# Performance work log

Hardware: AMD Instinct MI355X
Metric: run time of the kernel (lower is better)

## Reference

```python
import jax, jax.numpy as jnp
import numpy as np

B, T, D_IN, D_OUT = 4, 2048, 1024, 1024


def setup_inputs() -> dict:
    key = jax.random.key(0)
    k1, k2, k3, k4 = jax.random.split(key, 4)
    s_in = 1.0 / np.sqrt(D_IN)
    return {
        "input_vector": jax.random.normal(k1, (B, T, D_IN), dtype=jnp.float32),
        "w_q": jax.random.normal(k2, (D_IN, D_OUT), dtype=jnp.float32) * s_in,
        "w_k": jax.random.normal(k3, (D_IN, D_OUT), dtype=jnp.float32) * s_in,
        "w_v": jax.random.normal(k4, (D_IN, D_OUT), dtype=jnp.float32) * s_in,
    }


def reference(input_vector, w_q, w_k, w_v):
    # projections: [B, T, D_OUT]
    q = jnp.einsum("btd,de->bte", input_vector, w_q)
    k = jnp.einsum("btd,de->bte", input_vector, w_k)
    v = jnp.einsum("btd,de->bte", input_vector, w_v)

    T_ = q.shape[1]
    # raw scores [B, T, T]
    scores = jnp.einsum("bqd,bkd->bqk", q, k)
    # causal mask (strict upper triangle masked to -inf), applied BEFORE scaling
    # (as in the original; -inf is invariant under the scale anyway)
    causal = jnp.tril(jnp.ones((T_, T_), dtype=bool))  # True = keep
    scores = jnp.where(causal[None, :, :], scores, -jnp.inf)
    scores = scores / jnp.sqrt(jnp.asarray(k.shape[-1], scores.dtype))
    attn = jax.nn.softmax(scores, axis=-1)
    # dropout = 0.0 (eval): identity
    return jnp.einsum("bqk,bkd->bqd", attn, v)
```

## Files before the change

kernel.cpp:

```cpp
#include <hip/hip_runtime.h>
#include <cstdint>

typedef unsigned short u16;
typedef __attribute__((ext_vector_type(8))) short short8;
typedef __attribute__((ext_vector_type(16))) float f32x16;

__device__ __forceinline__ u16 f2bf(float f) {
  uint32_t u = __float_as_uint(f);
  u += 0x7FFFu + ((u >> 16) & 1u);
  return (u16)(u >> 16);
}

__device__ __forceinline__ void async_ld16(u16* lds, const u16* g) {
  __builtin_amdgcn_global_load_lds((const __attribute__((address_space(1))) uint32_t*)g,
                                   (__attribute__((address_space(3))) uint32_t*)lds,
                                   16, 0, 0);
}

__device__ __forceinline__ void lgkm0_fence() {
  asm volatile("s_waitcnt lgkmcnt(0)" ::: "memory");
  __builtin_amdgcn_sched_barrier(0);
}
__device__ __forceinline__ void vmw6_fence() {
  asm volatile("s_waitcnt vmcnt(6)" ::: "memory");
  __builtin_amdgcn_sched_barrier(0);
}
__device__ __forceinline__ void vmw0_fence() {
  asm volatile("s_waitcnt vmcnt(0)" ::: "memory");
  __builtin_amdgcn_sched_barrier(0);
}

#define MFMA32 __builtin_amdgcn_mfma_f32_32x32x16_bf16

template <int ROLE>
__global__ __launch_bounds__(512, 2) void g8(
    const u16* __restrict__ Xbf, const u16* __restrict__ Wt,
    u16* __restrict__ QK, u16* __restrict__ VtAll,
    u16* __restrict__ P, float* __restrict__ lpart)
{
  const int b = blockIdx.x;
  const int tid = threadIdx.x;
  const int lane = tid & 63;
  const int wave = tid >> 6;
  const int wr2 = wave >> 2;
  const int wc2 = wave & 3;
  const int m32 = lane & 31;
  const int hh = lane >> 5;

  __shared__ __align__(16) u16 ls[2][2][16384];

  const u16 *A, *B;
  u16* C = nullptr;
  long ldc = 1024;
  int m0, n0, zb = 0, nt = 0;

  if constexpr (ROLE == 0) {
    if (b < 256) {
      const int mat = b >> 7, v = b & 127;
      m0 = (v >> 2) * 256;
      n0 = (v & 3) * 256;
      A = Xbf;
      B = Wt + (long)mat * 1024 * 1024;
      C = QK + (long)mat * 8192 * 1024;
      ldc = 1024;
    } else {
      const int v = b - 256;
      m0 = (v >> 5) * 256;
      n0 = (v & 31) * 256;
      A = Wt + 2L * 1024 * 1024;
      B = Xbf;
      C = VtAll;
      ldc = 8192;
    }
  } else {
    zb = b / 36;
    const int w = b - zb * 36;
    int mt = 0;
    while ((mt + 1) * (mt + 2) / 2 <= w) ++mt;
    nt = w - mt * (mt + 1) / 2;
    m0 = mt * 256;
    n0 = nt * 256;
    A = QK + (long)zb * 2048 * 1024;
    B = QK + 8192L * 1024 + (long)zb * 2048 * 1024;
  }

  const int sr = tid >> 3, sg = tid & 7;
  const u16* pAst = A + (long)(m0 + sr) * 1024 + ((sg ^ (sr & 7)) * 8);
  const u16* pBst = B + (long)(n0 + sr) * 1024 + ((sg ^ (sr & 7)) * 8);

#define STG_A(bf, h, t_) do { \
    u16* _d = &ls[bf][0][(h) * 8192] + tid * 8; \
    const u16* _s = pAst + (long)(h) * 131072 + (long)(t_) * 64; \
    async_ld16(_d, _s); async_ld16(_d + 4096, _s + 65536); } while (0)
#define STG_B(bf, h, t_) do { \
    u16* _d = &ls[bf][1][(h) * 8192] + tid * 8; \
    const u16* _s = pBst + (long)(h) * 131072 + (long)(t_) * 64; \
    async_ld16(_d, _s); async_ld16(_d + 4096, _s + 65536); } while (0)

  int offAk[4], offBk[4];
#pragma unroll
  for (int ks = 0; ks < 4; ++ks) {
    const int kq = ((ks << 1) | hh) ^ (m32 & 7);
    offAk[ks] = (wr2 * 128 + m32) * 64 + kq * 8;
    offBk[ks] = (wc2 * 64 + m32) * 64 + kq * 8;
  }

  f32x16 acc[4][2];
#pragma unroll
  for (int i = 0; i < 4; ++i)
#pragma unroll
    for (int j = 0; j < 2; ++j)
#pragma unroll
      for (int r = 0; r < 16; ++r) acc[i][j][r] = 0.f;

  STG_A(0, 0, 0); STG_A(0, 1, 0); STG_B(0, 0, 0); STG_B(0, 1, 0);
  STG_B(1, 0, 1); STG_B(1, 1, 1); STG_A(1, 0, 1);
  vmw6_fence();
  __builtin_amdgcn_s_barrier();

  short8 A0[4], A1[4], A2[4], A3[4], B0r[4], B1r[4];

#pragma unroll 1
  for (int t = 0; t < 16; ++t) {
    const u16* la = ls[t & 1][0];
    const u16* lb = ls[t & 1][1];

#pragma unroll
    for (int ks = 0; ks < 4; ++ks) {
      A0[ks]  = *(const short8*)&la[offAk[ks]];
      A1[ks]  = *(const short8*)&la[offAk[ks] + 2048];
      B0r[ks] = *(const short8*)&lb[offBk[ks]];
    }
    if (t < 15) STG_A((t + 1) & 1, 1, t + 1);
    __builtin_amdgcn_s_barrier();
    lgkm0_fence();
    __builtin_amdgcn_s_setprio(1);
#pragma unroll
    for (int ks = 0; ks < 4; ++ks) {
      acc[0][0] = MFMA32(A0[ks], B0r[ks], acc[0][0], 0, 0, 0);
      acc[1][0] = MFMA32(A1[ks], B0r[ks], acc[1][0], 0, 0, 0);
    }
    __builtin_amdgcn_s_setprio(0);
    __builtin_amdgcn_s_barrier();

#pragma unroll
    for (int ks = 0; ks < 4; ++ks)
      B1r[ks] = *(const short8*)&lb[offBk[ks] + 2048];
    __builtin_amdgcn_s_barrier();
    lgkm0_fence();
    __builtin_amdgcn_s_setprio(1);
#pragma unroll
    for (int ks = 0; ks < 4; ++ks) {
      acc[0][1] = MFMA32(A0[ks], B1r[ks], acc[0][1], 0, 0, 0);
      acc[1][1] = MFMA32(A1[ks], B1r[ks], acc[1][1], 0, 0, 0);
    }
    __builtin_amdgcn_s_setprio(0);
    __builtin_amdgcn_s_barrier();

#pragma unroll
    for (int ks = 0; ks < 4; ++ks) {
      A2[ks] = *(const short8*)&la[offAk[ks] + 4096];
      A3[ks] = *(const short8*)&la[offAk[ks] + 6144];
    }
    if (t < 14) STG_B(t & 1, 0, t + 2);
    __builtin_amdgcn_s_barrier();
    lgkm0_fence();
    __builtin_amdgcn_s_setprio(1);
#pragma unroll
    for (int ks = 0; ks < 4; ++ks) {
      acc[2][0] = MFMA32(A2[ks], B0r[ks], acc[2][0], 0, 0, 0);
      acc[3][0] = MFMA32(A3[ks], B0r[ks], acc[3][0], 0, 0, 0);
    }
    __builtin_amdgcn_s_setprio(0);
    __builtin_amdgcn_s_barrier();

    if (t < 14) { STG_B(t & 1, 1, t + 2); STG_A(t & 1, 0, t + 2); }
    __builtin_amdgcn_s_barrier();
    __builtin_amdgcn_s_setprio(1);
#pragma unroll
    for (int ks = 0; ks < 4; ++ks) {
      acc[2][1] = MFMA32(A2[ks], B1r[ks], acc[2][1], 0, 0, 0);
      acc[3][1] = MFMA32(A3[ks], B1r[ks], acc[3][1], 0, 0, 0);
    }
    __builtin_amdgcn_s_setprio(0);
    if (t < 14) vmw6_fence(); else vmw0_fence();
    __builtin_amdgcn_s_barrier();
  }
#undef STG_A
#undef STG_B

  const int ec = lane & 31;
  const int rb = hh * 4;

  if constexpr (ROLE == 0) {
#pragma unroll
    for (int i = 0; i < 4; ++i) {
      const int rbase = m0 + wr2 * 128 + i * 32 + rb;
#pragma unroll
      for (int j = 0; j < 2; ++j) {
        const int col = n0 + wc2 * 64 + j * 32 + ec;
#pragma unroll
        for (int r = 0; r < 16; ++r) {
          const int row = rbase + (r & 3) + 8 * (r >> 2);
          C[(long)row * ldc + col] = f2bf(acc[i][j][r]);
        }
      }
    }
  } else {
    u16* Cp = P + (long)zb * 2048 * 2048;
    float* lp = lpart + (long)zb * 32 * 2048 + (long)(nt * 4 + wc2) * 2048;
#pragma unroll
    for (int i = 0; i < 4; ++i) {
      const int rbl = wr2 * 128 + i * 32 + rb;
      float rsum[16];
#pragma unroll
      for (int r = 0; r < 16; ++r) rsum[r] = 0.f;
#pragma unroll
      for (int j = 0; j < 2; ++j) {
        const int col = n0 + wc2 * 64 + j * 32 + ec;
#pragma unroll
        for (int r = 0; r < 16; ++r) {
          const int row = m0 + rbl + (r & 3) + 8 * (r >> 2);
          float pv = __expf(acc[i][j][r] * 0.03125f);
          if (col > row) pv = 0.f;
          Cp[(long)row * 2048 + col] = f2bf(pv);
          rsum[r] += pv;
        }
      }
#pragma unroll
      for (int r = 0; r < 16; ++r) {
        float s = rsum[r];
#pragma unroll
        for (int off = 1; off < 32; off <<= 1) s += __shfl_xor(s, off, 64);
        if ((lane & 31) == 0)
          lp[m0 + rbl + (r & 3) + 8 * (r >> 2)] = s;
      }
    }
  }
}

template <int ROLE>
__global__ __launch_bounds__(256) void gk(
    const u16* __restrict__ Xbf, const u16* __restrict__ Wt,
    u16* __restrict__ QK, u16* __restrict__ VtAll,
    u16* __restrict__ P, float* __restrict__ lpart,
    float* __restrict__ out)
{
  const int b = blockIdx.x;
  const int tid = threadIdx.x;
  const int lane = tid & 63;
  const int wave = tid >> 6;
  const int wr = (wave >> 1) * 64;
  const int wc = (wave & 1) * 64;

  __shared__ __align__(16) u16 ls[4][4096];
  __shared__ float l_s[128];

  const int c0 = tid, c1 = tid + 256;
  const int r0 = c0 >> 2, q0 = ((c0 & 3) ^ ((c0 >> 3) & 3)) * 8;
  const int r1 = c1 >> 2, q1 = ((c1 & 3) ^ ((c1 >> 3) & 3)) * 8;

  const int m32 = lane & 31;
  const int hh = lane >> 5;
  const int rsw = (m32 >> 1) & 3;
  int offA[2][2], offB[2][2];
#pragma unroll
  for (int i = 0; i < 2; ++i)
#pragma unroll
    for (int ks = 0; ks < 2; ++ks) {
      const int kq = ((ks << 1) | hh) ^ rsw;
      offA[i][ks] = (wr + i * 32 + m32) * 32 + kq * 8;
      offB[i][ks] = (wc + i * 32 + m32) * 32 + kq * 8;
    }

  const u16 *A, *B;
  int lda, ldb, kmax, m0, n0, mb, nb, zb = 0;
  const int u = b & 7, idx = b >> 3;
  zb = blockIdx.y;
  if (idx < 8) { mb = 15 - u; nb = idx; }
  else         { mb = u;      nb = idx - 8; }
  A = P + (long)zb * 2048 * 2048; lda = 2048;
  B = VtAll + (long)zb * 2048; ldb = 8192;
  kmax = (mb + 1) * 128;
  m0 = mb * 128;
  n0 = nb * 128;

  const u16* pA0 = A + (long)(m0 + r0) * lda + q0;
  const u16* pA1 = A + (long)(m0 + r1) * lda + q1;
  const u16* pB0 = B + (long)(n0 + r0) * ldb + q0;
  const u16* pB1 = B + (long)(n0 + r1) * ldb + q1;

  f32x16 acc[2][2];
#pragma unroll
  for (int i = 0; i < 2; ++i)
#pragma unroll
    for (int j = 0; j < 2; ++j)
#pragma unroll
      for (int r = 0; r < 16; ++r) acc[i][j][r] = 0.f;

  async_ld16(&ls[0][c0 * 8], pA0);
  async_ld16(&ls[0][c1 * 8], pA1);
  async_ld16(&ls[2][c0 * 8], pB0);
  async_ld16(&ls[2][c1 * 8], pB1);
  pA0 += 32; pA1 += 32; pB0 += 32; pB1 += 32;

  int p = 0;
  for (int k0 = 0; k0 < kmax; k0 += 32) {
    __syncthreads();
    if (k0 + 32 < kmax) {
      u16* la = ls[p ^ 1];
      u16* lb = ls[2 + (p ^ 1)];
      async_ld16(&la[c0 * 8], pA0);
      async_ld16(&la[c1 * 8], pA1);
      async_ld16(&lb[c0 * 8], pB0);
      async_ld16(&lb[c1 * 8], pB1);
      pA0 += 32; pA1 += 32; pB0 += 32; pB1 += 32;
    }

    const u16* la = ls[p];
    const u16* lb = ls[2 + p];
#pragma unroll
    for (int ks = 0; ks < 2; ++ks) {
      const short8 a0 = *(const short8*)&la[offA[0][ks]];
      const short8 a1 = *(const short8*)&la[offA[1][ks]];
      const short8 b0 = *(const short8*)&lb[offB[0][ks]];
      const short8 b1 = *(const short8*)&lb[offB[1][ks]];
      acc[0][0] = MFMA32(a0, b0, acc[0][0], 0, 0, 0);
      acc[0][1] = MFMA32(a0, b1, acc[0][1], 0, 0, 0);
      acc[1][0] = MFMA32(a1, b0, acc[1][0], 0, 0, 0);
      acc[1][1] = MFMA32(a1, b1, acc[1][1], 0, 0, 0);
    }
    p ^= 1;
  }

  const int ec = lane & 31;
  const int rb = (lane >> 5) * 4;

  __syncthreads();
  if (tid < 128) {
    const float* lp = lpart + (long)zb * 32 * 2048 + m0 + tid;
    float s0 = 0.f, s1 = 0.f;
    const int nch = 2 * (mb + 1);
    for (int c = 0; c < nch; c += 2) {
      s0 += lp[(long)c * 2048];
      s1 += lp[(long)(c + 1) * 2048];
    }
    l_s[tid] = 1.f / (s0 + s1);
  }
  __syncthreads();
  float* Cf = out + (long)zb * 2048 * 1024;
#pragma unroll
  for (int i = 0; i < 2; ++i) {
    const int rbl = wr + i * 32 + rb;
#pragma unroll
    for (int j = 0; j < 2; ++j) {
      const int col = n0 + wc + j * 32 + ec;
#pragma unroll
      for (int r = 0; r < 16; ++r) {
        const int rl = rbl + (r & 3) + 8 * (r >> 2);
        Cf[(long)(m0 + rl) * 1024 + col] = acc[i][j][r] * l_s[rl];
      }
    }
  }
}

__global__ __launch_bounds__(256) void cast_fused(
    const float* __restrict__ x, const float* __restrict__ w0,
    const float* __restrict__ w1, const float* __restrict__ w2,
    u16* __restrict__ Xbf, u16* __restrict__ Wt)
{
  const int b = blockIdx.x;
  if (b < 8192) {
    const long i = ((long)b * 256 + threadIdx.x) * 4;
    const float4 v = *(const float4*)(x + i);
    ushort4 o;
    o.x = f2bf(v.x); o.y = f2bf(v.y); o.z = f2bf(v.z); o.w = f2bf(v.w);
    *(ushort4*)(Xbf + i) = o;
  } else {
    const int bb = b - 8192;
    const int z = bb >> 10, rem = bb & 1023;
    const float* W = (z == 0) ? w0 : (z == 1) ? w1 : w2;
    u16* o = Wt + (long)z * 1024 * 1024;
    __shared__ float t[32][33];
    const int n0 = (rem & 31) * 32, k0 = (rem >> 5) * 32;
    const int tx = threadIdx.x & 31, ty = threadIdx.x >> 5;
    for (int r = ty; r < 32; r += 8) t[r][tx] = W[(long)(k0 + r) * 1024 + n0 + tx];
    __syncthreads();
    for (int r = ty; r < 32; r += 8) o[(long)(n0 + r) * 1024 + k0 + tx] = f2bf(t[tx][r]);
  }
}

extern "C" void kernel_launch(void* const* d_in, const int* in_sizes, int n_in,
                              void* d_out, int out_size, void* d_ws, size_t ws_size,
                              hipStream_t stream) {
  const float* X  = (const float*)d_in[0];
  const float* Wq = (const float*)d_in[1];
  const float* Wk = (const float*)d_in[2];
  const float* Wv = (const float*)d_in[3];
  float* out = (float*)d_out;

  u16* Xbf   = (u16*)d_ws;
  u16* Wt    = Xbf + 8192L * 1024;
  u16* QK    = Wt + 3L * 1024 * 1024;
  u16* VtAll = QK + 2L * 8192 * 1024;
  u16* P     = VtAll + 1024L * 8192;
  float* lpart = (float*)(P + 4L * 2048 * 2048);

  cast_fused<<<8192 + 3072, 256, 0, stream>>>(X, Wq, Wk, Wv, Xbf, Wt);

  g8<0><<<384, 512, 0, stream>>>(Xbf, Wt, QK, VtAll, P, lpart);

  g8<1><<<144, 512, 0, stream>>>(Xbf, Wt, QK, VtAll, P, lpart);

  gk<2><<<dim3(128, 4), 256, 0, stream>>>(Xbf, Wt, QK, VtAll, P, lpart, out);
}
```

Before: 255.3 us.

## Rebalance kernels: fuse Q/K projection tiles, co-schedule V with scores, shrink PV tiles

The Q and K projections now share one A tile of X per block, each block loading both weight matrices, so X is read once for both outputs. The V-transpose projection moves into the scores launch, so the 144 causal score blocks and 128 V blocks run together and fill the GPU better. Score tiles are computed transposed so P can be written with 4-wide vector stores, and the row-sum partials shrink to one per 128-key chunk. The PV kernel uses 128x64 output tiles ordered heaviest-first to improve occupancy and load balance, at the cost of re-reading P once more per extra column tile.

```diff
diff --git a/kernel.cpp b/kernel.cpp
--- a/kernel.cpp
+++ b/kernel.cpp
@@ -49,44 +49,49 @@
 
   __shared__ __align__(16) u16 ls[2][2][16384];
 
-  const u16 *A, *B;
-  u16* C = nullptr;
-  long ldc = 1024;
-  int m0, n0, zb = 0, nt = 0;
+  const u16 *Abase, *Bh0, *Bh1;
+  int m0, n0, zb = 0;
+  bool scoresRole = false;
 
   if constexpr (ROLE == 0) {
-    if (b < 256) {
-      const int mat = b >> 7, v = b & 127;
-      m0 = (v >> 2) * 256;
-      n0 = (v & 3) * 256;
-      A = Xbf;
-      B = Wt + (long)mat * 1024 * 1024;
-      C = QK + (long)mat * 8192 * 1024;
-      ldc = 1024;
+    m0 = (b >> 3) * 256;
+    n0 = (b & 7) * 128;
+    Abase = Xbf;
+    Bh0 = Wt;
+    Bh1 = Wt + 1024L * 1024;
+  } else {
+    if (b < 144) {
+      scoresRole = true;
+      zb = b / 36;
+      const int w = b - zb * 36;
+      int mt = 0;
+      while ((mt + 1) * (mt + 2) / 2 <= w) ++mt;
+      const int nt = w - mt * (mt + 1) / 2;
+      m0 = nt * 256;
+      n0 = mt * 256;
+      Abase = QK + 8192L * 1024 + (long)zb * 2048 * 1024;
+      const u16* Bq = QK + (long)zb * 2048 * 1024;
+      Bh0 = Bq; Bh1 = Bq;
     } else {
-      const int v = b - 256;
+      const int v = b - 144;
       m0 = (v >> 5) * 256;
       n0 = (v & 31) * 256;
-      A = Wt + 2L * 1024 * 1024;
-      B = Xbf;
-      C = VtAll;
-      ldc = 8192;
-    }
+      Abase = Wt + 2L * 1024 * 1024;
+      Bh0 = Xbf; Bh1 = Xbf;
+    }
+  }
+
+  const int sr = tid >> 3, sg = tid & 7;
+  const long swz = (long)((sg ^ (sr & 7)) * 8);
+  const u16* pAst = Abase + (long)(m0 + sr) * 1024 + swz;
+  const u16* pB[2];
+  if constexpr (ROLE == 0) {
+    pB[0] = Bh0 + (long)(n0 + sr) * 1024 + swz;
+    pB[1] = Bh1 + (long)(n0 + sr) * 1024 + swz;
   } else {
-    zb = b / 36;
-    const int w = b - zb * 36;
-    int mt = 0;
-    while ((mt + 1) * (mt + 2) / 2 <= w) ++mt;
-    nt = w - mt * (mt + 1) / 2;
-    m0 = mt * 256;
-    n0 = nt * 256;
-    A = QK + (long)zb * 2048 * 1024;
-    B = QK + 8192L * 1024 + (long)zb * 2048 * 1024;
-  }
-
-  const int sr = tid >> 3, sg = tid & 7;
-  const u16* pAst = A + (long)(m0 + sr) * 1024 + ((sg ^ (sr & 7)) * 8);
-  const u16* pBst = B + (long)(n0 + sr) * 1024 + ((sg ^ (sr & 7)) * 8);
+    pB[0] = Bh0 + (long)(n0 + sr) * 1024 + swz;
+    pB[1] = Bh0 + (long)(n0 + 128 + sr) * 1024 + swz;
+  }
 
 #define STG_A(bf, h, t_) do { \
     u16* _d = &ls[bf][0][(h) * 8192] + tid * 8; \
@@ -94,15 +99,20 @@
     async_ld16(_d, _s); async_ld16(_d + 4096, _s + 65536); } while (0)
 #define STG_B(bf, h, t_) do { \
     u16* _d = &ls[bf][1][(h) * 8192] + tid * 8; \
-    const u16* _s = pBst + (long)(h) * 131072 + (long)(t_) * 64; \
+    const u16* _s = pB[h] + (long)(t_) * 64; \
     async_ld16(_d, _s); async_ld16(_d + 4096, _s + 65536); } while (0)
 
-  int offAk[4], offBk[4];
+  int offAk[4], offBk[2][4];
 #pragma unroll
   for (int ks = 0; ks < 4; ++ks) {
     const int kq = ((ks << 1) | hh) ^ (m32 & 7);
     offAk[ks] = (wr2 * 128 + m32) * 64 + kq * 8;
-    offBk[ks] = (wc2 * 64 + m32) * 64 + kq * 8;
+#pragma unroll
+    for (int j = 0; j < 2; ++j) {
+      const int rowB = (ROLE == 0) ? (j * 128 + wc2 * 32 + m32)
+                                   : (wc2 * 64 + j * 32 + m32);
+      offBk[j][ks] = rowB * 64 + kq * 8;
+    }
   }
 
   f32x16 acc[4][2];
@@ -129,7 +139,7 @@
     for (int ks = 0; ks < 4; ++ks) {
       A0[ks]  = *(const short8*)&la[offAk[ks]];
       A1[ks]  = *(const short8*)&la[offAk[ks] + 2048];
-      B0r[ks] = *(const short8*)&lb[offBk[ks]];
+      B0r[ks] = *(const short8*)&lb[offBk[0][ks]];
     }
     if (t < 15) STG_A((t + 1) & 1, 1, t + 1);
     __builtin_amdgcn_s_barrier();
@@ -145,7 +155,7 @@
 
 #pragma unroll
     for (int ks = 0; ks < 4; ++ks)
-      B1r[ks] = *(const short8*)&lb[offBk[ks] + 2048];
+      B1r[ks] = *(const short8*)&lb[offBk[1][ks]];
     __builtin_amdgcn_s_barrier();
     lgkm0_fence();
     __builtin_amdgcn_s_setprio(1);
@@ -194,6 +204,52 @@
 
   if constexpr (ROLE == 0) {
 #pragma unroll
+    for (int j = 0; j < 2; ++j) {
+      u16* Cj = QK + (long)j * 8192 * 1024;
+      const int col = n0 + wc2 * 32 + ec;
+#pragma unroll
+      for (int i = 0; i < 4; ++i) {
+        const int rbase = m0 + wr2 * 128 + i * 32 + rb;
+#pragma unroll
+        for (int r = 0; r < 16; ++r) {
+          const int row = rbase + (r & 3) + 8 * (r >> 2);
+          Cj[(long)row * 1024 + col] = f2bf(acc[i][j][r]);
+        }
+      }
+    }
+  } else if (scoresRole) {
+    u16* Pp = P + (long)zb * 2048 * 2048;
+    float* lpz = lpart + (long)zb * 16 * 2048;
+    const int chunk = (m0 >> 7) + wr2;
+#pragma unroll
+    for (int j = 0; j < 2; ++j) {
+      const int q = n0 + wc2 * 64 + j * 32 + ec;
+      float s = 0.f;
+#pragma unroll
+      for (int i = 0; i < 4; ++i) {
+        const int kb = m0 + wr2 * 128 + i * 32 + rb;
+#pragma unroll
+        for (int u = 0; u < 4; ++u) {
+          const int k0r = kb + u * 8;
+          float pv[4];
+#pragma unroll
+          for (int v = 0; v < 4; ++v) {
+            float e = __expf(acc[i][j][u * 4 + v] * 0.03125f);
+            if (k0r + v > q) e = 0.f;
+            pv[v] = e;
+            s += e;
+          }
+          ushort4 o;
+          o.x = f2bf(pv[0]); o.y = f2bf(pv[1]);
+          o.z = f2bf(pv[2]); o.w = f2bf(pv[3]);
+          *(ushort4*)&Pp[(long)q * 2048 + k0r] = o;
+        }
+      }
+      s += __shfl_xor(s, 32, 64);
+      if (hh == 0) lpz[(long)chunk * 2048 + q] = s;
+    }
+  } else {
+#pragma unroll
     for (int i = 0; i < 4; ++i) {
       const int rbase = m0 + wr2 * 128 + i * 32 + rb;
 #pragma unroll
@@ -202,59 +258,37 @@
 #pragma unroll
         for (int r = 0; r < 16; ++r) {
           const int row = rbase + (r & 3) + 8 * (r >> 2);
-          C[(long)row * ldc + col] = f2bf(acc[i][j][r]);
+          VtAll[(long)row * 8192 + col] = f2bf(acc[i][j][r]);
         }
       }
     }
-  } else {
-    u16* Cp = P + (long)zb * 2048 * 2048;
-    float* lp = lpart + (long)zb * 32 * 2048 + (long)(nt * 4 + wc2) * 2048;
-#pragma unroll
-    for (int i = 0; i < 4; ++i) {
-      const int rbl = wr2 * 128 + i * 32 + rb;
-      float rsum[16];
-#pragma unroll
-      for (int r = 0; r < 16; ++r) rsum[r] = 0.f;
-#pragma unroll
-      for (int j = 0; j < 2; ++j) {
-        const int col = n0 + wc2 * 64 + j * 32 + ec;
-#pragma unroll
-        for (int r = 0; r < 16; ++r) {
-          const int row = m0 + rbl + (r & 3) + 8 * (r >> 2);
-          float pv = __expf(acc[i][j][r] * 0.03125f);
-          if (col > row) pv = 0.f;
-          Cp[(long)row * 2048 + col] = f2bf(pv);
-          rsum[r] += pv;
-        }
-      }
-#pragma unroll
-      for (int r = 0; r < 16; ++r) {
-        float s = rsum[r];
-#pragma unroll
-        for (int off = 1; off < 32; off <<= 1) s += __shfl_xor(s, off, 64);
-        if ((lane & 31) == 0)
-          lp[m0 + rbl + (r & 3) + 8 * (r >> 2)] = s;
-      }
-    }
-  }
-}
-
-template <int ROLE>
-__global__ __launch_bounds__(256) void gk(
-    const u16* __restrict__ Xbf, const u16* __restrict__ Wt,
-    u16* __restrict__ QK, u16* __restrict__ VtAll,
-    u16* __restrict__ P, float* __restrict__ lpart,
-    float* __restrict__ out)
+  }
+}
+
+__global__ __launch_bounds__(256) void pv(
+    const u16* __restrict__ VtAll, const u16* __restrict__ P,
+    const float* __restrict__ lpart, float* __restrict__ out)
 {
   const int b = blockIdx.x;
   const int tid = threadIdx.x;
   const int lane = tid & 63;
   const int wave = tid >> 6;
   const int wr = (wave >> 1) * 64;
-  const int wc = (wave & 1) * 64;
-
-  __shared__ __align__(16) u16 ls[4][4096];
+  const int wc = (wave & 1) * 32;
+
+  __shared__ __align__(16) u16 lsa[2][4096];
+  __shared__ __align__(16) u16 lsb[2][2048];
   __shared__ float l_s[128];
+
+  const int zb = blockIdx.y;
+  const int mb = 15 - (b >> 4);
+  const int nb = b & 15;
+  const int m0 = mb * 128;
+  const int n0 = nb * 64;
+  const int kmax = (mb + 1) * 128;
+
+  const u16* A = P + (long)zb * 2048 * 2048;
+  const u16* B = VtAll + (long)zb * 2048;
 
   const int c0 = tid, c1 = tid + 256;
   const int r0 = c0 >> 2, q0 = ((c0 & 3) ^ ((c0 >> 3) & 3)) * 8;
@@ -263,103 +297,74 @@
   const int m32 = lane & 31;
   const int hh = lane >> 5;
   const int rsw = (m32 >> 1) & 3;
-  int offA[2][2], offB[2][2];
+  int offA[2][2], offB[2];
+#pragma unroll
+  for (int ks = 0; ks < 2; ++ks) {
+    const int kq = ((ks << 1) | hh) ^ rsw;
+#pragma unroll
+    for (int i = 0; i < 2; ++i)
+      offA[i][ks] = (wr + i * 32 + m32) * 32 + kq * 8;
+    offB[ks] = (wc + m32) * 32 + kq * 8;
+  }
+
+  const u16* pA0 = A + (long)(m0 + r0) * 2048 + q0;
+  const u16* pA1 = A + (long)(m0 + r1) * 2048 + q1;
+  const u16* pB0 = B + (long)(n0 + r0) * 8192 + q0;
+
+  f32x16 acc[2];
 #pragma unroll
   for (int i = 0; i < 2; ++i)
 #pragma unroll
-    for (int ks = 0; ks < 2; ++ks) {
-      const int kq = ((ks << 1) | hh) ^ rsw;
-      offA[i][ks] = (wr + i * 32 + m32) * 32 + kq * 8;
-      offB[i][ks] = (wc + i * 32 + m32) * 32 + kq * 8;
-    }
-
-  const u16 *A, *B;
-  int lda, ldb, kmax, m0, n0, mb, nb, zb = 0;
-  const int u = b & 7, idx = b >> 3;
-  zb = blockIdx.y;
-  if (idx < 8) { mb = 15 - u; nb = idx; }
-  else         { mb = u;      nb = idx - 8; }
-  A = P + (long)zb * 2048 * 2048; lda = 2048;
-  B = VtAll + (long)zb * 2048; ldb = 8192;
-  kmax = (mb + 1) * 128;
-  m0 = mb * 128;
-  n0 = nb * 128;
-
-  const u16* pA0 = A + (long)(m0 + r0) * lda + q0;
-  const u16* pA1 = A + (long)(m0 + r1) * lda + q1;
-  const u16* pB0 = B + (long)(n0 + r0) * ldb + q0;
-  const u16* pB1 = B + (long)(n0 + r1) * ldb + q1;
-
-  f32x16 acc[2][2];
-#pragma unroll
-  for (int i = 0; i < 2; ++i)
-#pragma unroll
-    for (int j = 0; j < 2; ++j)
-#pragma unroll
-      for (int r = 0; r < 16; ++r) acc[i][j][r] = 0.f;
-
-  async_ld16(&ls[0][c0 * 8], pA0);
-  async_ld16(&ls[0][c1 * 8], pA1);
-  async_ld16(&ls[2][c0 * 8], pB0);
-  async_ld16(&ls[2][c1 * 8], pB1);
-  pA0 += 32; pA1 += 32; pB0 += 32; pB1 += 32;
+    for (int r = 0; r < 16; ++r) acc[i][r] = 0.f;
+
+  async_ld16(&lsa[0][c0 * 8], pA0);
+  async_ld16(&lsa[0][c1 * 8], pA1);
+  async_ld16(&lsb[0][c0 * 8], pB0);
+  pA0 += 32; pA1 += 32; pB0 += 32;
 
   int p = 0;
   for (int k0 = 0; k0 < kmax; k0 += 32) {
     __syncthreads();
     if (k0 + 32 < kmax) {
-      u16* la = ls[p ^ 1];
-      u16* lb = ls[2 + (p ^ 1)];
-      async_ld16(&la[c0 * 8], pA0);
-      async_ld16(&la[c1 * 8], pA1);
-      async_ld16(&lb[c0 * 8], pB0);
-      async_ld16(&lb[c1 * 8], pB1);
-      pA0 += 32; pA1 += 32; pB0 += 32; pB1 += 32;
-    }
-
-    const u16* la = ls[p];
-    const u16* lb = ls[2 + p];
+      async_ld16(&lsa[p ^ 1][c0 * 8], pA0);
+      async_ld16(&lsa[p ^ 1][c1 * 8], pA1);
+      async_ld16(&lsb[p ^ 1][c0 * 8], pB0);
+      pA0 += 32; pA1 += 32; pB0 += 32;
+    }
+    const u16* la = lsa[p];
+    const u16* lb = lsb[p];
 #pragma unroll
     for (int ks = 0; ks < 2; ++ks) {
       const short8 a0 = *(const short8*)&la[offA[0][ks]];
       const short8 a1 = *(const short8*)&la[offA[1][ks]];
-      const short8 b0 = *(const short8*)&lb[offB[0][ks]];
-      const short8 b1 = *(const short8*)&lb[offB[1][ks]];
-      acc[0][0] = MFMA32(a0, b0, acc[0][0], 0, 0, 0);
-      acc[0][1] = MFMA32(a0, b1, acc[0][1], 0, 0, 0);
-      acc[1][0] = MFMA32(a1, b0, acc[1][0], 0, 0, 0);
-      acc[1][1] = MFMA32(a1, b1, acc[1][1], 0, 0, 0);
+      const short8 bb = *(const short8*)&lb[offB[ks]];
+      acc[0] = MFMA32(a0, bb, acc[0], 0, 0, 0);
+      acc[1] = MFMA32(a1, bb, acc[1], 0, 0, 0);
     }
     p ^= 1;
   }
-
-  const int ec = lane & 31;
-  const int rb = (lane >> 5) * 4;
 
   __syncthreads();
   if (tid < 128) {
-    const float* lp = lpart + (long)zb * 32 * 2048 + m0 + tid;
-    float s0 = 0.f, s1 = 0.f;
-    const int nch = 2 * (mb + 1);
-    for (int c = 0; c < nch; c += 2) {
-      s0 += lp[(long)c * 2048];
-      s1 += lp[(long)(c + 1) * 2048];
-    }
-    l_s[tid] = 1.f / (s0 + s1);
+    const float* lp = lpart + (long)zb * 16 * 2048 + m0 + tid;
+    float s = 0.f;
+    const int nch = (mb | 1) + 1;
+    for (int c = 0; c < nch; ++c) s += lp[(long)c * 2048];
+    l_s[tid] = 1.f / s;
   }
   __syncthreads();
+
+  const int ec = lane & 31;
+  const int rb = hh * 4;
   float* Cf = out + (long)zb * 2048 * 1024;
 #pragma unroll
   for (int i = 0; i < 2; ++i) {
     const int rbl = wr + i * 32 + rb;
-#pragma unroll
-    for (int j = 0; j < 2; ++j) {
-      const int col = n0 + wc + j * 32 + ec;
-#pragma unroll
-      for (int r = 0; r < 16; ++r) {
-        const int rl = rbl + (r & 3) + 8 * (r >> 2);
-        Cf[(long)(m0 + rl) * 1024 + col] = acc[i][j][r] * l_s[rl];
-      }
+    const int col = n0 + wc + ec;
+#pragma unroll
+    for (int r = 0; r < 16; ++r) {
+      const int rl = rbl + (r & 3) + 8 * (r >> 2);
+      Cf[(long)(m0 + rl) * 1024 + col] = acc[i][r] * l_s[rl];
     }
   }
 }
@@ -408,9 +413,9 @@
 
   cast_fused<<<8192 + 3072, 256, 0, stream>>>(X, Wq, Wk, Wv, Xbf, Wt);
 
-  g8<0><<<384, 512, 0, stream>>>(Xbf, Wt, QK, VtAll, P, lpart);
-
-  g8<1><<<144, 512, 0, stream>>>(Xbf, Wt, QK, VtAll, P, lpart);
-
-  gk<2><<<dim3(128, 4), 256, 0, stream>>>(Xbf, Wt, QK, VtAll, P, lpart, out);
-}
+  g8<0><<<256, 512, 0, stream>>>(Xbf, Wt, QK, VtAll, P, lpart);
+
+  g8<1><<<272, 512, 0, stream>>>(Xbf, Wt, QK, VtAll, P, lpart);
+
+  pv<<<dim3(256, 4), 256, 0, stream>>>(VtAll, P, lpart, out);
+}
```

Result: no change. 258.3 us (+1.2%).
